# Kernel tuning notes

Hardware: AMD Instinct MI355X
Metric: run time of the kernel (lower is better)

## Reference

```python
import jax, jax.numpy as jnp
import numpy as np
from jax import lax

H = 128; N = 32768; D = 16; B = 256; E2 = N * D; L = 2; NC = 10
NPG = N // B  # nodes per graph


def _ln(x, g, b):
    m = jnp.mean(x, -1, keepdims=True)
    v = jnp.mean((x - m) ** 2, -1, keepdims=True)
    return (x - m) * lax.rsqrt(v + 1e-5) * g + b


def _lrelu(x):
    return jnp.where(x >= 0, x, 0.01 * x)


def _seg_mean(x, ids):
    s = jax.ops.segment_sum(x, ids, num_segments=B)
    c = jax.ops.segment_sum(jnp.ones((x.shape[0], 1), x.dtype), ids, num_segments=B)
    return s / c


def _lstm_agg(seq, Wih, Whh, bih, bhh):
    # seq: [N, D, H] neighbor message sequences; returns final hidden [N, H]
    n = seq.shape[0]
    h0 = jnp.zeros((n, H), seq.dtype)

    def step(carry, x):
        h, c = carry
        g = x @ Wih.T + bih + h @ Whh.T + bhh  # [N, 4H], gate order i,f,g,o (torch LSTM)
        i, f, gg, o = jnp.split(g, 4, axis=-1)
        c = jax.nn.sigmoid(f) * c + jax.nn.sigmoid(i) * jnp.tanh(gg)
        h = jax.nn.sigmoid(o) * jnp.tanh(c)
        return (h, c), None

    (h, _), _ = lax.scan(step, (h0, h0), jnp.swapaxes(seq, 0, 1))
    return h


def _gru(x, h, Wih, Whh, bih, bhh):
    gi = x @ Wih.T + bih
    gh = h @ Whh.T + bhh
    ir, iz, inn = jnp.split(gi, 3, axis=-1)
    hr, hz, hn = jnp.split(gh, 3, axis=-1)
    r = jax.nn.sigmoid(ir + hr)
    z = jax.nn.sigmoid(iz + hz)
    nn_ = jnp.tanh(inn + r * hn)
    return (1.0 - z) * nn_ + z * h


def _sage(fs, fd, nbr, Wih, Whh, bih, bhh, fsW, fsb, fnW, fnb):
    # SAGEConv with LSTM aggregator: fc_self(dst) + fc_neigh(lstm over neighbor feats)
    hn = _lstm_agg(fs[nbr], Wih, Whh, bih, bhh)  # [N, H]
    return fd @ fsW.T + fsb + hn @ fnW.T + fnb


def _forward(ints, fl):
    (act_ids, dur_ids, act2_ids, nbr_a2d, nbr_d2a, src2, dst2, graph_ids) = ints
    (emb_act, emb_dur, emb_act2, transform_W, transform_b,
     ggc_W, ggc_b, gru_Wih, gru_Whh, gru_bih, gru_bhh, hn_g, hn_b,
     lstm_Wih, lstm_Whh, lstm_bih, lstm_bhh, fcs_W, fcs_b, fcn_W, fcn_b,
     n1_g, n1_b, n3_g, n3_b,
     mh_W1, mh_b1, mh_W2, mh_b2, mo_W1, mo_b1, mo_W2, mo_b2,
     mlp_W1, mlp_b1, mlp_W2, mlp_b2, cls_W, cls_b) = fl

    # embedding lookups (dropout layers are identity in eval mode)
    h_act = emb_act[act_ids]
    h_dur = emb_dur[dur_ids]
    h_g2 = emb_act2[act2_ids]
    h_new = jnp.concatenate([h_g2, h_dur], axis=1) @ transform_W.T + transform_b

    # homo branch: GatedGraphConv (n_steps=2, 1 etype) + residual + LN + leaky_relu
    res = h_new
    hh = h_new
    for _ in range(2):
        m = hh @ ggc_W.T + ggc_b
        a = jax.ops.segment_sum(m[src2], dst2, num_segments=N)
        hh = _gru(a, hh, gru_Wih, gru_Whh, gru_bih, gru_bhh)
    h_new = _lrelu(_ln(hh + res, hn_g, hn_b))
    hg2_mean = _seg_mean(h_new, graph_ids)  # [B, H]

    # hetero branch: L layers of HeteroGraphConv(SAGEConv lstm) + norms + residuals
    ha, hd = h_act, h_dur
    for l in range(L):
        nd = _sage(ha, hd, nbr_a2d, lstm_Wih[l, 0], lstm_Whh[l, 0], lstm_bih[l, 0], lstm_bhh[l, 0],
                   fcs_W[l, 0], fcs_b[l, 0], fcn_W[l, 0], fcn_b[l, 0])
        na = _sage(hd, ha, nbr_d2a, lstm_Wih[l, 1], lstm_Whh[l, 1], lstm_bih[l, 1], lstm_bhh[l, 1],
                   fcs_W[l, 1], fcs_b[l, 1], fcn_W[l, 1], fcn_b[l, 1])
        na = _lrelu(_ln(na, n1_g[l, 0], n1_b[l, 0]))
        nd = _lrelu(_ln(nd, n1_g[l, 1], n1_b[l, 1]))
        ha = _lrelu(_ln(ha + na, n3_g[l, 0], n3_b[l, 0]))
        hd = _lrelu(_ln(hd + nd, n3_g[l, 1], n3_b[l, 1]))
    hg_mean = _seg_mean(ha, graph_ids) + _seg_mean(hd, graph_ids)  # sum over ntypes

    o1 = jax.nn.relu(jax.nn.relu(hg2_mean @ mo_W1.T + mo_b1) @ mo_W2.T + mo_b2)
    o2 = jax.nn.relu(jax.nn.relu(hg_mean @ mh_W1.T + mh_b1) @ mh_W2.T + mh_b2)
    hc = jnp.concatenate([o1, hg2_mean, o2, hg_mean], axis=1)  # [B, 4H]
    preds = jax.nn.relu(jax.nn.relu(hc @ mlp_W1.T + mlp_b1) @ mlp_W2.T + mlp_b2)
    return preds @ cls_W.T + cls_b  # [B, NC]


def setup_inputs() -> dict:
    key = jax.random.key(0)
    ks = iter(jax.random.split(key, 48))
    s = 1.0 / np.sqrt(H)

    def nrm(shape, sc=s):
        return jax.random.normal(next(ks), shape, jnp.float32) * sc

    inp = {}
    inp['act_ids'] = jax.random.randint(next(ks), (N,), 0, 30)
    inp['dur_ids'] = jax.random.randint(next(ks), (N,), 0, 1024)
    inp['act2_ids'] = jax.random.randint(next(ks), (N,), 0, 30)
    inp['nbr_a2d'] = jax.random.randint(next(ks), (N, D), 0, N)
    inp['nbr_d2a'] = jax.random.randint(next(ks), (N, D), 0, N)
    inp['src2'] = jax.random.randint(next(ks), (E2,), 0, N)
    inp['dst2'] = jax.random.randint(next(ks), (E2,), 0, N)
    inp['graph_ids'] = jnp.arange(N) // NPG

    inp['emb_act'] = nrm((30, H))
    inp['emb_dur'] = nrm((1024, H))
    inp['emb_act2'] = nrm((30, H))
    inp['transform_W'] = nrm((H, 2 * H), 1.0 / np.sqrt(2 * H))
    inp['transform_b'] = jnp.zeros((H,), jnp.float32)
    inp['ggc_W'] = nrm((H, H))
    inp['ggc_b'] = jnp.zeros((H,), jnp.float32)
    inp['gru_Wih'] = nrm((3 * H, H))
    inp['gru_Whh'] = nrm((3 * H, H))
    inp['gru_bih'] = jnp.zeros((3 * H,), jnp.float32)
    inp['gru_bhh'] = jnp.zeros((3 * H,), jnp.float32)
    inp['hn_g'] = jnp.ones((H,), jnp.float32)
    inp['hn_b'] = jnp.zeros((H,), jnp.float32)
    inp['lstm_Wih'] = nrm((L, 2, 4 * H, H))
    inp['lstm_Whh'] = nrm((L, 2, 4 * H, H))
    inp['lstm_bih'] = jnp.zeros((L, 2, 4 * H), jnp.float32)
    inp['lstm_bhh'] = jnp.zeros((L, 2, 4 * H), jnp.float32)
    inp['fcs_W'] = nrm((L, 2, H, H))
    inp['fcs_b'] = jnp.zeros((L, 2, H), jnp.float32)
    inp['fcn_W'] = nrm((L, 2, H, H))
    inp['fcn_b'] = jnp.zeros((L, 2, H), jnp.float32)
    inp['n1_g'] = jnp.ones((L, 2, H), jnp.float32)
    inp['n1_b'] = jnp.zeros((L, 2, H), jnp.float32)
    inp['n3_g'] = jnp.ones((L, 2, H), jnp.float32)
    inp['n3_b'] = jnp.zeros((L, 2, H), jnp.float32)
    inp['mh_W1'] = nrm((H, H)); inp['mh_b1'] = jnp.zeros((H,), jnp.float32)
    inp['mh_W2'] = nrm((H, H)); inp['mh_b2'] = jnp.zeros((H,), jnp.float32)
    inp['mo_W1'] = nrm((H, H)); inp['mo_b1'] = jnp.zeros((H,), jnp.float32)
    inp['mo_W2'] = nrm((H, H)); inp['mo_b2'] = jnp.zeros((H,), jnp.float32)
    inp['mlp_W1'] = nrm((2 * H, 4 * H), 1.0 / np.sqrt(4 * H))
    inp['mlp_b1'] = jnp.zeros((2 * H,), jnp.float32)
    inp['mlp_W2'] = nrm((H, 2 * H), 1.0 / np.sqrt(2 * H))
    inp['mlp_b2'] = jnp.zeros((H,), jnp.float32)
    inp['cls_W'] = nrm((NC, H))
    inp['cls_b'] = jnp.zeros((NC,), jnp.float32)
    return inp


def reference(act_ids, dur_ids, act2_ids, nbr_a2d, nbr_d2a, src2, dst2, graph_ids,
              emb_act, emb_dur, emb_act2, transform_W, transform_b,
              ggc_W, ggc_b, gru_Wih, gru_Whh, gru_bih, gru_bhh, hn_g, hn_b,
              lstm_Wih, lstm_Whh, lstm_bih, lstm_bhh, fcs_W, fcs_b, fcn_W, fcn_b,
              n1_g, n1_b, n3_g, n3_b,
              mh_W1, mh_b1, mh_W2, mh_b2, mo_W1, mo_b1, mo_W2, mo_b2,
              mlp_W1, mlp_b1, mlp_W2, mlp_b2, cls_W, cls_b):
    ints = (act_ids, dur_ids, act2_ids, nbr_a2d, nbr_d2a, src2, dst2, graph_ids)
    fl = (emb_act, emb_dur, emb_act2, transform_W, transform_b,
          ggc_W, ggc_b, gru_Wih, gru_Whh, gru_bih, gru_bhh, hn_g, hn_b,
          lstm_Wih, lstm_Whh, lstm_bih, lstm_bhh, fcs_W, fcs_b, fcn_W, fcn_b,
          n1_g, n1_b, n3_g, n3_b,
          mh_W1, mh_b1, mh_W2, mh_b2, mo_W1, mo_b1, mo_W2, mo_b2,
          mlp_W1, mlp_b1, mlp_W2, mlp_b2, cls_W, cls_b)
    return _forward(ints, fl)
```

## Files before the change

### kernel.cpp

```cpp
#include <hip/hip_runtime.h>
#include <hip/hip_fp16.h>
#include <math.h>

#define NN 32768
#define HH 128
#define DD 16
#define BB 256
#define E2N (NN*DD)
#define NF (NN*HH)

typedef __attribute__((ext_vector_type(4))) float f32x4;
typedef __attribute__((ext_vector_type(4))) unsigned short u16x4;
typedef __attribute__((ext_vector_type(8))) unsigned short u16x8;
typedef _Float16 f16x8 __attribute__((ext_vector_type(8)));

__device__ __forceinline__ float fsig(float x) {
  return __builtin_amdgcn_rcpf(1.0f + __builtin_amdgcn_exp2f(-1.442695041f*x));
}
__device__ __forceinline__ float ftanh(float x) {
  return 1.0f - 2.0f*__builtin_amdgcn_rcpf(1.0f + __builtin_amdgcn_exp2f(2.885390082f*x));
}

struct TDesc { const float* src; float* dst; int R; int C; };
struct TDescArr { TDesc d[8]; };

__global__ void transpose_many(TDescArr da) {
  TDesc t = da.d[blockIdx.y];
  int idx = blockIdx.x*256 + threadIdx.x;
  if (idx < t.R*t.C) {
    int r = idx / t.C, c = idx - r*t.C;
    t.dst[(size_t)c*t.R + r] = t.src[idx];
  }
}

__global__ void bias_sum_kernel(const float* __restrict__ bih, const float* __restrict__ bhh,
                                float* __restrict__ bsum) {
  int i = blockIdx.x*256 + threadIdx.x;
  if (i < 2048) bsum[i] = bih[i] + bhh[i];
}

__global__ void f32to16_kernel(const float* __restrict__ in, unsigned short* __restrict__ out) {
  int base = (blockIdx.x*256 + threadIdx.x) * 4;
  float4 v = *(const float4*)(in + base);
  u16x4 p;
  p[0] = __half_as_ushort(__float2half_rn(v.x));
  p[1] = __half_as_ushort(__float2half_rn(v.y));
  p[2] = __half_as_ushort(__float2half_rn(v.z));
  p[3] = __half_as_ushort(__float2half_rn(v.w));
  *(u16x4*)(out + base) = p;
}

__global__ void hist_kernel(const int* __restrict__ dst, int* __restrict__ cnt) {
  int e = blockIdx.x*256 + threadIdx.x;
  atomicAdd(&cnt[dst[e]], 1);
}

__global__ __launch_bounds__(1024) void scan_kernel(const int* __restrict__ cnt,
                                                    int* __restrict__ rowptr,
                                                    int* __restrict__ cursor) {
  __shared__ int part[1024];
  const int t = threadIdx.x;
  const int base = t*32;
  int loc[32];
  int s = 0;
#pragma unroll
  for (int k=0;k<32;++k){ loc[k]=s; s += cnt[base+k]; }
  part[t] = s;
  __syncthreads();
  for (int off=1; off<1024; off<<=1) {
    int v = (t>=off) ? part[t-off] : 0;
    __syncthreads();
    part[t] += v;
    __syncthreads();
  }
  int pbase = part[t] - s;
#pragma unroll
  for (int k=0;k<32;++k){ int v = pbase + loc[k]; rowptr[base+k]=v; cursor[base+k]=v; }
  if (t == 1023) rowptr[NN] = part[1023];
}

__global__ void fill_kernel(const int* __restrict__ src, const int* __restrict__ dst,
                            int* __restrict__ cursor, int* __restrict__ elist) {
  int e = blockIdx.x*256 + threadIdx.x;
  int p = atomicAdd(&cursor[dst[e]], 1);
  elist[p] = src[e];
}

__global__ __launch_bounds__(256) void gather_ggc(const float* __restrict__ m,
    const int* __restrict__ rowptr, const int* __restrict__ elist,
    float* __restrict__ a) {
  const int node = blockIdx.x*4 + (threadIdx.x>>6);
  const int lane = threadIdx.x & 63;
  const int s0 = rowptr[node], s1 = rowptr[node+1];
  float a0 = 0.0f, a1 = 0.0f;
  for (int e=s0; e<s1; ++e) {
    const float* mr = m + (size_t)elist[e]*128;
    a0 += mr[lane];
    a1 += mr[64+lane];
  }
  float* ar = a + (size_t)node*128;
  ar[lane] = a0;
  ar[64+lane] = a1;
}

__global__ void embed3_kernel(const int* __restrict__ a_ids, const int* __restrict__ d_ids,
                              const int* __restrict__ a2_ids,
                              const float* __restrict__ ea, const float* __restrict__ ed,
                              const float* __restrict__ ea2,
                              float* __restrict__ ha, float* __restrict__ hd,
                              float* __restrict__ hg2,
                              unsigned short* __restrict__ fs16a,
                              unsigned short* __restrict__ fs16d) {
  int idx = blockIdx.x*256 + threadIdx.x;
  int n = idx >> 7, j = idx & 127;
  int w = blockIdx.y;
  if (w == 0) {
    float v = ea[(size_t)a_ids[n]*128 + j];
    ha[idx] = v;
    fs16a[idx] = __half_as_ushort(__float2half_rn(v));
  } else if (w == 1) {
    float v = ed[(size_t)d_ids[n]*128 + j];
    hd[idx] = v;
    fs16d[idx] = __half_as_ushort(__float2half_rn(v));
  } else {
    hg2[idx] = ea2[(size_t)a2_ids[n]*128 + j];
  }
}

template<int BN, int ACT>
__global__ __launch_bounds__(256) void gemm_nt(
    const float* __restrict__ A0, const float* __restrict__ A1,
    const float* __restrict__ A2, const float* __restrict__ A3,
    int lda, const float* __restrict__ WT, const float* __restrict__ bias,
    float* __restrict__ C, int K, int beta)
{
  extern __shared__ float sm[];
  const int KP = K + 4;
  float* At = sm;
  float* Bc = sm + 32*KP;
  const int tid = threadIdx.x;
  const int m0 = blockIdx.x*32;
  const int ng = tid >> 5, cg = tid & 31;
  const int n0 = ng*4, c4 = cg*4;
  constexpr int G = BN/128;
  float acc[G][4][4];
#pragma unroll
  for (int g=0; g<G; ++g)
#pragma unroll
    for (int i=0;i<4;++i)
#pragma unroll
      for (int e=0;e<4;++e) acc[g][i][e] = 0.0f;

  const int nf4 = K >> 2;
  for (int idx = tid; idx < 32*nf4; idx += 256) {
    int row = idx / nf4;
    int kk = (idx - row*nf4) << 2;
    const float* Ap = (kk < 128) ? A0 : (kk < 256) ? A1 : (kk < 384) ? A2 : A3;
    float4 v = *(const float4*)(Ap + (size_t)(m0+row)*lda + (kk & 127));
    *(float4*)(At + row*KP + kk) = v;
  }
  const int nchunk = K >> 4;
  for (int kc = 0; kc < nchunk; ++kc) {
    __syncthreads();
    for (int idx = tid; idx < 16*(BN/4); idx += 256) {
      int kk = idx / (BN/4);
      int jq = idx - kk*(BN/4);
      *(float4*)(Bc + kk*BN + jq*4) = *(const float4*)(WT + (size_t)(kc*16+kk)*BN + jq*4);
    }
    __syncthreads();
    for (int k=0;k<16;++k) {
      const int kk = kc*16 + k;
      float av[4];
#pragma unroll
      for (int i=0;i<4;++i) av[i] = At[(n0+i)*KP + kk];
#pragma unroll
      for (int g=0; g<G; ++g) {
        float4 bv = *(const float4*)(Bc + k*BN + g*128 + c4);
        float bb[4] = {bv.x, bv.y, bv.z, bv.w};
#pragma unroll
        for (int i=0;i<4;++i)
#pragma unroll
          for (int e=0;e<4;++e)
            acc[g][i][e] += av[i]*bb[e];
      }
    }
  }
#pragma unroll
  for (int g=0; g<G; ++g) {
#pragma unroll
    for (int i=0;i<4;++i) {
      float* dst = C + (size_t)(m0+n0+i)*BN + g*128 + c4;
      float o[4];
#pragma unroll
      for (int e=0;e<4;++e) o[e] = acc[g][i][e];
      if (bias) {
#pragma unroll
        for (int e=0;e<4;++e) o[e] += bias[g*128 + c4 + e];
      }
      if (beta) {
        float4 p = *(const float4*)dst;
        o[0]+=p.x; o[1]+=p.y; o[2]+=p.z; o[3]+=p.w;
      }
      if (ACT==1) {
#pragma unroll
        for (int e=0;e<4;++e) o[e] = fmaxf(o[e], 0.0f);
      }
      *(float4*)dst = make_float4(o[0],o[1],o[2],o[3]);
    }
  }
}

__device__ __forceinline__ void stage_f16(const float* __restrict__ A, int rb, int tid,
                                          unsigned short* x16) {
  const int r = tid >> 3;
  const int cf = (tid & 7) * 16;
  const float* src = A + (size_t)(rb + r)*128 + cf;
  unsigned short* d = x16 + r*136 + cf;
#pragma unroll
  for (int q=0; q<4; ++q) {
    float4 v = *(const float4*)(src + q*4);
    u16x4 p;
    p[0] = __half_as_ushort(__float2half_rn(v.x));
    p[1] = __half_as_ushort(__float2half_rn(v.y));
    p[2] = __half_as_ushort(__float2half_rn(v.z));
    p[3] = __half_as_ushort(__float2half_rn(v.w));
    *(u16x4*)(d + q*4) = p;
  }
}

__global__ __launch_bounds__(512) void mgemm(
    const float* __restrict__ A, const unsigned short* __restrict__ W16,
    const float* __restrict__ bias, float* __restrict__ C, int BN, int ntpw)
{
  __shared__ unsigned short x16[64*136];
  const int tid = threadIdx.x;
  const int w = tid >> 6;
  const int lane = tid & 63;
  const int ln16 = lane & 15;
  const int lq = lane >> 4;
  const int rb = blockIdx.x * 64;
  stage_f16(A, rb, tid, x16);
  __syncthreads();

  for (int j=0; j<ntpw; ++j) {
    const int tile = w + j*8;
    f32x4 acc[4];
    f32x4 bv = *(const f32x4*)(bias + tile*16 + lq*4);
#pragma unroll
    for (int nt=0; nt<4; ++nt) acc[nt] = bv;
#pragma unroll
    for (int kt=0; kt<4; ++kt) {
      const int bo = kt*32 + lq*8;
      f16x8 bx[4];
#pragma unroll
      for (int nt=0; nt<4; ++nt)
        bx[nt] = *(const f16x8*)(x16 + (nt*16+ln16)*136 + bo);
      f16x8 ah = *(const f16x8*)(W16 + (size_t)(tile*16 + ln16)*128 + kt*32 + lq*8);
#pragma unroll
      for (int nt=0; nt<4; ++nt)
        acc[nt] = __builtin_amdgcn_mfma_f32_16x16x32_f16(ah, bx[nt], acc[nt], 0,0,0);
    }
#pragma unroll
    for (int nt=0; nt<4; ++nt) {
      f32x4 o = acc[nt];
      *(float4*)(C + (size_t)(rb + nt*16 + ln16)*BN + tile*16 + lq*4) =
          make_float4(o[0],o[1],o[2],o[3]);
    }
  }
}

__global__ __launch_bounds__(512) void mgemm2(
    const float* __restrict__ A1, const unsigned short* __restrict__ W1,
    const float* __restrict__ A2, const unsigned short* __restrict__ W2,
    const float* __restrict__ bias1, const float* __restrict__ bias2,
    float* __restrict__ C, float* __restrict__ C2, int wstride)
{
  __shared__ unsigned short x1[64*136];
  __shared__ unsigned short x2[64*136];
  const int tid = threadIdx.x;
  const int w = tid >> 6;
  const int lane = tid & 63;
  const int ln16 = lane & 15;
  const int lq = lane >> 4;
  const int rb = blockIdx.x * 64;
  stage_f16(A1, rb, tid, x1);
  stage_f16(A2, rb, tid, x2);
  __syncthreads();

  f32x4 acc[4];
  {
    f32x4 bv = *(const f32x4*)(bias1 + w*16 + lq*4);
    if (bias2) {
      f32x4 b2 = *(const f32x4*)(bias2 + w*16 + lq*4);
#pragma unroll
      for (int e=0;e<4;++e) bv[e] += b2[e];
    }
#pragma unroll
    for (int nt=0; nt<4; ++nt) acc[nt] = bv;
  }
#pragma unroll
  for (int p=0; p<2; ++p) {
    const unsigned short* x = p ? x2 : x1;
    const unsigned short* W = p ? W2 : W1;
#pragma unroll
    for (int kt=0; kt<4; ++kt) {
      const int bo = kt*32 + lq*8;
      f16x8 bx[4];
#pragma unroll
      for (int nt=0; nt<4; ++nt)
        bx[nt] = *(const f16x8*)(x + (nt*16+ln16)*136 + bo);
      f16x8 ah = *(const f16x8*)(W + (size_t)(w*16 + ln16)*wstride + kt*32 + lq*8);
#pragma unroll
      for (int nt=0; nt<4; ++nt)
        acc[nt] = __builtin_amdgcn_mfma_f32_16x16x32_f16(ah, bx[nt], acc[nt], 0,0,0);
    }
  }
#pragma unroll
  for (int nt=0; nt<4; ++nt) {
    f32x4 o = acc[nt];
    const size_t off = (size_t)(rb + nt*16 + ln16)*128 + w*16 + lq*4;
    *(float4*)(C + off) = make_float4(o[0],o[1],o[2],o[3]);
    if (C2) *(float4*)(C2 + off) = make_float4(o[0],o[1],o[2],o[3]);
  }
}

__global__ __launch_bounds__(512) void gru_fused(
    const float* __restrict__ abuf, float* __restrict__ hh,
    const unsigned short* __restrict__ GI16, const unsigned short* __restrict__ GH16,
    const float* __restrict__ bih, const float* __restrict__ bhh)
{
  __shared__ unsigned short x16[64*136];
  __shared__ unsigned short h16[64*136];
  const int tid = threadIdx.x;
  const int w = tid >> 6;
  const int lane = tid & 63;
  const int ln16 = lane & 15;
  const int lq = lane >> 4;
  const int rb = blockIdx.x * 64;
  stage_f16(abuf, rb, tid, x16);
  stage_f16(hh, rb, tid, h16);
  __syncthreads();

  f32x4 rr[4], zz[4], nn_[4];
#pragma unroll
  for (int j=0; j<3; ++j) {
    const int tile = w + j*8;
    f32x4 ai[4], ag[4];
    f32x4 bi = *(const f32x4*)(bih + tile*16 + lq*4);
    f32x4 bg = *(const f32x4*)(bhh + tile*16 + lq*4);
#pragma unroll
    for (int nt=0; nt<4; ++nt) { ai[nt] = bi; ag[nt] = bg; }
#pragma unroll
    for (int kt=0; kt<4; ++kt) {
      const int bo = kt*32 + lq*8;
      f16x8 bx[4], bh_[4];
#pragma unroll
      for (int nt=0; nt<4; ++nt) {
        bx[nt] = *(const f16x8*)(x16 + (nt*16+ln16)*136 + bo);
        bh_[nt] = *(const f16x8*)(h16 + (nt*16+ln16)*136 + bo);
      }
      const size_t co = (size_t)(tile*16 + ln16)*128 + kt*32 + lq*8;
      f16x8 aI = *(const f16x8*)(GI16 + co);
      f16x8 aH = *(const f16x8*)(GH16 + co);
#pragma unroll
      for (int nt=0; nt<4; ++nt) {
        ai[nt] = __builtin_amdgcn_mfma_f32_16x16x32_f16(aI, bx[nt], ai[nt], 0,0,0);
        ag[nt] = __builtin_amdgcn_mfma_f32_16x16x32_f16(aH, bh_[nt], ag[nt], 0,0,0);
      }
    }
#pragma unroll
    for (int nt=0; nt<4; ++nt) {
#pragma unroll
      for (int e=0; e<4; ++e) {
        if (j == 0)      rr[nt][e] = fsig(ai[nt][e] + ag[nt][e]);
        else if (j == 1) zz[nt][e] = fsig(ai[nt][e] + ag[nt][e]);
        else             nn_[nt][e] = ftanh(ai[nt][e] + rr[nt][e]*ag[nt][e]);
      }
    }
  }
#pragma unroll
  for (int nt=0; nt<4; ++nt) {
    float* hp = hh + (size_t)(rb + nt*16 + ln16)*128 + w*16 + lq*4;
    float4 ho = *(const float4*)hp;
    float hv[4] = {ho.x, ho.y, ho.z, ho.w};
    float o[4];
#pragma unroll
    for (int e=0; e<4; ++e)
      o[e] = (1.0f - zz[nt][e])*nn_[nt][e] + zz[nt][e]*hv[e];
    *(float4*)hp = make_float4(o[0],o[1],o[2],o[3]);
  }
}

__global__ __launch_bounds__(512) void lstm_fused6(
    float* __restrict__ hL,
    const unsigned short* __restrict__ fs16a, const unsigned short* __restrict__ fs16d,
    const int* __restrict__ nbrA, const int* __restrict__ nbrD,
    const unsigned short* __restrict__ WI0, const unsigned short* __restrict__ WH0,
    const unsigned short* __restrict__ WI1, const unsigned short* __restrict__ WH1,
    const float* __restrict__ bsum0, const float* __restrict__ bsum1)
{
  __shared__ unsigned short xb[64*132];
  __shared__ unsigned short hb[64*132];
  const int tid = threadIdx.x;
  const int w = tid >> 6;
  const int lane = tid & 63;
  const int ln16 = lane & 15;
  const int lq = lane >> 4;
  const int b = blockIdx.x;
  const bool dir = (b >= 512);
  const int nb = (dir ? (b - 512) : b) * 64;
  const unsigned short* fs16 = dir ? fs16d : fs16a;
  const int* nbr = dir ? nbrD : nbrA;
  const unsigned short* WI = dir ? WI1 : WI0;
  const unsigned short* WH = dir ? WH1 : WH0;
  const float* bsum = dir ? bsum1 : bsum0;

  const int gr = tid >> 3;
  const int gc = (tid & 7) * 16;
  const int* nrow = nbr + (size_t)(nb + gr)*DD;

  f32x4 bias[4];
#pragma unroll
  for (int g=0; g<4; ++g)
    bias[g] = *(const f32x4*)(bsum + g*128 + w*16 + lq*4);

  f32x4 cst[4];
#pragma unroll
  for (int nt=0; nt<4; ++nt)
#pragma unroll
    for (int e=0; e<4; ++e) cst[nt][e] = 0.0f;

  u16x8 xg0, xg1;
  {
    int gidx = nrow[0];
    const unsigned short* src = fs16 + (size_t)gidx*128 + gc;
    xg0 = *(const u16x8*)(src);
    xg1 = *(const u16x8*)(src + 8);
    unsigned short* d = xb + gr*132 + gc;
    *(u16x8*)d = xg0;
    *(u16x8*)(d+8) = xg1;
  }
  int gnext = nrow[1];

#pragma unroll 1
  for (int t=0; t<16; ++t) {
    __syncthreads();

    f32x4 racc[4][4];
#pragma unroll
    for (int g=0; g<4; ++g)
#pragma unroll
      for (int nt=0; nt<4; ++nt)
        racc[g][nt] = bias[g];

#pragma unroll
    for (int kt=0; kt<4; ++kt) {
      const int bo = kt*32 + lq*8;
      f16x8 bx[4];
#pragma unroll
      for (int nt=0; nt<4; ++nt)
        bx[nt] = *(const f16x8*)(xb + (nt*16+ln16)*132 + bo);
#pragma unroll
      for (int g=0; g<4; ++g) {
        f16x8 aI = *(const f16x8*)(WI + (size_t)(g*128 + w*16 + ln16)*128 + kt*32 + lq*8);
#pragma unroll
        for (int nt=0; nt<4; ++nt)
          racc[g][nt] = __builtin_amdgcn_mfma_f32_16x16x32_f16(aI, bx[nt], racc[g][nt], 0,0,0);
      }
    }
    if (t < 15) {
      const unsigned short* src = fs16 + (size_t)gnext*128 + gc;
      xg0 = *(const u16x8*)(src);
      xg1 = *(const u16x8*)(src + 8);
      if (t < 14) gnext = nrow[t+2];
    }
    if (t > 0) {
#pragma unroll
      for (int kt=0; kt<4; ++kt) {
        const int bo = kt*32 + lq*8;
        f16x8 bh[4];
#pragma unroll
        for (int nt=0; nt<4; ++nt)
          bh[nt] = *(const f16x8*)(hb + (nt*16+ln16)*132 + bo);
#pragma unroll
        for (int g=0; g<4; ++g) {
          f16x8 aH = *(const f16x8*)(WH + (size_t)(g*128 + w*16 + ln16)*128 + kt*32 + lq*8);
#pragma unroll
          for (int nt=0; nt<4; ++nt)
            racc[g][nt] = __builtin_amdgcn_mfma_f32_16x16x32_f16(aH, bh[nt], racc[g][nt], 0,0,0);
        }
      }
    }
    __syncthreads();

#pragma unroll
    for (int nt=0; nt<4; ++nt) {
      float hv[4];
#pragma unroll
      for (int e=0; e<4; ++e) {
        float ig = fsig(racc[0][nt][e]);
        float fg = fsig(racc[1][nt][e]);
        float gg = ftanh(racc[2][nt][e]);
        float og = fsig(racc[3][nt][e]);
        float cc = fg*cst[nt][e] + ig*gg;
        cst[nt][e] = cc;
        hv[e] = og*ftanh(cc);
      }
      const int node = nt*16 + ln16;
      const int col = w*16 + lq*4;
      if (t < 15) {
        u16x4 hw;
#pragma unroll
        for (int e=0; e<4; ++e) hw[e] = __half_as_ushort(__float2half_rn(hv[e]));
        *(u16x4*)(hb + node*132 + col) = hw;
      } else {
        *(float4*)(hL + (size_t)((dir?NN:0) + nb + node)*128 + col) =
            make_float4(hv[0], hv[1], hv[2], hv[3]);
      }
    }
    if (t < 15) {
      unsigned short* d = xb + gr*132 + gc;
      *(u16x8*)d = xg0;
      *(u16x8*)(d+8) = xg1;
    }
  }
}

__global__ void ln_lrelu_kernel(float* __restrict__ out, const float* __restrict__ x,
                                const float* __restrict__ add,
                                const float* __restrict__ g, const float* __restrict__ b) {
  int n = blockIdx.x, j = threadIdx.x;
  size_t base = (size_t)n*128;
  float v = x[base+j];
  if (add) v += add[base+j];
  __shared__ float sh[4];
  float s = v;
#pragma unroll
  for (int m=32; m>=1; m>>=1) s += __shfl_xor(s, m, 64);
  if ((j&63)==0) sh[j>>6] = s;
  __syncthreads();
  float mean = (sh[0]+sh[1]) * 0.0078125f;
  float d = v - mean;
  float q = d*d;
#pragma unroll
  for (int m=32; m>=1; m>>=1) q += __shfl_xor(q, m, 64);
  if ((j&63)==0) sh[2+(j>>6)] = q;
  __syncthreads();
  float var = (sh[2]+sh[3]) * 0.0078125f;
  float y = d * rsqrtf(var + 1e-5f) * g[j] + b[j];
  out[base+j] = (y >= 0.0f) ? y : 0.01f*y;
}

__global__ void ln13_kernel(float* __restrict__ h, const float* __restrict__ nsrc,
                            const float* __restrict__ g1, const float* __restrict__ b1,
                            const float* __restrict__ g3, const float* __restrict__ b3,
                            unsigned short* __restrict__ out16) {
  int n = blockIdx.x, j = threadIdx.x;
  size_t base = (size_t)n*128;
  __shared__ float sh[4];
  float v = nsrc[base+j];
  float s = v;
#pragma unroll
  for (int m=32; m>=1; m>>=1) s += __shfl_xor(s, m, 64);
  if ((j&63)==0) sh[j>>6] = s;
  __syncthreads();
  float mean = (sh[0]+sh[1]) * 0.0078125f;
  float d = v - mean;
  float q = d*d;
#pragma unroll
  for (int m=32; m>=1; m>>=1) q += __shfl_xor(q, m, 64);
  if ((j&63)==0) sh[2+(j>>6)] = q;
  __syncthreads();
  float var = (sh[2]+sh[3]) * 0.0078125f;
  float y1 = d * rsqrtf(var + 1e-5f) * g1[j] + b1[j];
  y1 = (y1 >= 0.0f) ? y1 : 0.01f*y1;
  __syncthreads();
  float u = h[base+j] + y1;
  s = u;
#pragma unroll
  for (int m=32; m>=1; m>>=1) s += __shfl_xor(s, m, 64);
  if ((j&63)==0) sh[j>>6] = s;
  __syncthreads();
  mean = (sh[0]+sh[1]) * 0.0078125f;
  d = u - mean;
  q = d*d;
#pragma unroll
  for (int m=32; m>=1; m>>=1) q += __shfl_xor(q, m, 64);
  if ((j&63)==0) sh[2+(j>>6)] = q;
  __syncthreads();
  var = (sh[2]+sh[3]) * 0.0078125f;
  float y3 = d * rsqrtf(var + 1e-5f) * g3[j] + b3[j];
  float o = (y3 >= 0.0f) ? y3 : 0.01f*y3;
  h[base+j] = o;
  if (out16) out16[base+j] = __half_as_ushort(__float2half_rn(o));
}

__global__ void segmean_kernel(float* __restrict__ out, const float* __restrict__ x,
                               const float* __restrict__ y) {
  int b = blockIdx.x, j = threadIdx.x;
  float s = 0.0f;
  for (int r=0; r<128; ++r) {
    size_t n = (size_t)(b*128 + r)*128 + j;
    s += x[n];
    if (y) s += y[n];
  }
  out[(size_t)b*128 + j] = s * 0.0078125f;
}

__global__ void cls_kernel(float* __restrict__ out, const float* __restrict__ h2,
                           const float* __restrict__ Wc, const float* __restrict__ bc) {
  int gid = blockIdx.x*256 + threadIdx.x;
  if (gid >= BB*10) return;
  int mrow = gid/10, c = gid - mrow*10;
  const float* arow = h2 + (size_t)mrow*128;
  const float* wrow = Wc + (size_t)c*128;
  float s = bc[c];
  for (int k=0;k<128;++k) s += arow[k]*wrow[k];
  out[gid] = s;
}

__global__ void bail_kernel(float* out, float v) {
  if (threadIdx.x==0 && blockIdx.x==0) out[0] = v;
}

extern "C" void kernel_launch(void* const* d_in, const int* in_sizes, int n_in,
                              void* d_out, int out_size, void* d_ws, size_t ws_size,
                              hipStream_t stream)
{
  const int* act_ids  = (const int*)d_in[0];
  const int* dur_ids  = (const int*)d_in[1];
  const int* act2_ids = (const int*)d_in[2];
  const int* nbr_a2d  = (const int*)d_in[3];
  const int* nbr_d2a  = (const int*)d_in[4];
  const int* src2     = (const int*)d_in[5];
  const int* dst2     = (const int*)d_in[6];
  const float* emb_act     = (const float*)d_in[8];
  const float* emb_dur     = (const float*)d_in[9];
  const float* emb_act2    = (const float*)d_in[10];
  const float* transform_W = (const float*)d_in[11];
  const float* transform_b = (const float*)d_in[12];
  const float* ggc_W   = (const float*)d_in[13];
  const float* ggc_b   = (const float*)d_in[14];
  const float* gru_Wih = (const float*)d_in[15];
  const float* gru_Whh = (const float*)d_in[16];
  const float* gru_bih = (const float*)d_in[17];
  const float* gru_bhh = (const float*)d_in[18];
  const float* hn_g    = (const float*)d_in[19];
  const float* hn_b    = (const float*)d_in[20];
  const float* lstm_Wih = (const float*)d_in[21];
  const float* lstm_Whh = (const float*)d_in[22];
  const float* lstm_bih = (const float*)d_in[23];
  const float* lstm_bhh = (const float*)d_in[24];
  const float* fcs_W = (const float*)d_in[25];
  const float* fcs_b = (const float*)d_in[26];
  const float* fcn_W = (const float*)d_in[27];
  const float* fcn_b = (const float*)d_in[28];
  const float* n1_g = (const float*)d_in[29];
  const float* n1_b = (const float*)d_in[30];
  const float* n3_g = (const float*)d_in[31];
  const float* n3_b = (const float*)d_in[32];
  const float* mh_W1 = (const float*)d_in[33];
  const float* mh_b1 = (const float*)d_in[34];
  const float* mh_W2 = (const float*)d_in[35];
  const float* mh_b2 = (const float*)d_in[36];
  const float* mo_W1 = (const float*)d_in[37];
  const float* mo_b1 = (const float*)d_in[38];
  const float* mo_W2 = (const float*)d_in[39];
  const float* mo_b2 = (const float*)d_in[40];
  const float* mlp_W1 = (const float*)d_in[41];
  const float* mlp_b1 = (const float*)d_in[42];
  const float* mlp_W2 = (const float*)d_in[43];
  const float* mlp_b2 = (const float*)d_in[44];
  const float* cls_W = (const float*)d_in[45];
  const float* cls_b = (const float*)d_in[46];

  float* ws = (float*)d_ws;
  float* ha   = ws;
  float* hd   = ws + (size_t)NF;
  float* hg2  = ws + 2*(size_t)NF;
  float* res  = ws + 3*(size_t)NF;
  float* hh   = ws + 4*(size_t)NF;
  float* SCR  = ws + 5*(size_t)NF;
  float* mb   = SCR;
  float* abuf = SCR + (size_t)NF;
  float* hnf  = mb;
  float* hLb  = SCR + 8*(size_t)NF;
  float* SMALL = ws + 15*(size_t)NF;
  float* hg2m = SMALL;
  float* hgm  = SMALL + 32768;
  float* o1b  = SMALL + 65536;
  float* o2b  = SMALL + 98304;
  float* t1b  = SMALL + 131072;
  float* t2b  = SMALL + 163840;
  float* h1b  = SMALL + 196608;
  float* h2b  = SMALL + 262144;
  float* bsum = SMALL + 294912;
  float* WTb  = SMALL + 296960;
  const size_t NEED_BYTES = (size_t)(15*(size_t)NF + 296960 + 1032192) * 4;
  if (ws_size < NEED_BYTES) {
    hipMemsetAsync(d_out, 0, (size_t)out_size*sizeof(float), stream);
    bail_kernel<<<1,64,0,stream>>>((float*)d_out, (float)ws_size);
    return;
  }
  float* na = hg2;
  float* nd = res;
  unsigned short* fs16a = (unsigned short*)(SCR + 2*(size_t)NF);
  unsigned short* fs16d = fs16a + (size_t)NF;
  int* csr_cnt    = (int*)(SCR + 3*(size_t)NF);
  int* csr_rowptr = csr_cnt + NN;
  int* csr_cursor = csr_rowptr + NN + 2;
  int* csr_elist  = csr_cursor + NN;

  const int O_TRANSFORM = 0;
  const int O_SPLIT    = 147456;
  const int O_SPLIT2   = 409600;
  const int O_MH1      = 802816;
  const int O_MH2      = 819200;
  const int O_MO1      = 835584;
  const int O_MO2      = 851968;
  const int O_MLP1     = 868352;
  const int O_MLP2     = 999424;

  unsigned short* T16 = (unsigned short*)(WTb + O_TRANSFORM);
  unsigned short* WI16 = (unsigned short*)(WTb + O_SPLIT);
  unsigned short* WH16 = WI16 + 4*65536;

  unsigned short* SP2 = (unsigned short*)(WTb + O_SPLIT2);
  unsigned short* GGC16 = SP2;
  unsigned short* GIH16 = GGC16 + 16384;
  unsigned short* GHH16 = GIH16 + 49152;
  unsigned short* FCS16 = GHH16 + 49152;
  unsigned short* FCN16 = FCS16 + 65536;

  TDescArr da;
  int di = 0;
  auto addT = [&](const float* s, float* d, int R, int C){ da.d[di].src=s; da.d[di].dst=d; da.d[di].R=R; da.d[di].C=C; ++di; };
  addT(mh_W1, WTb + O_MH1, 128, 128);
  addT(mh_W2, WTb + O_MH2, 128, 128);
  addT(mo_W1, WTb + O_MO1, 128, 128);
  addT(mo_W2, WTb + O_MO2, 128, 128);
  addT(mlp_W1, WTb + O_MLP1, 256, 512);
  addT(mlp_W2, WTb + O_MLP2, 128, 256);
  transpose_many<<<dim3(512, di), 256, 0, stream>>>(da);
  bias_sum_kernel<<<8, 256, 0, stream>>>(lstm_bih, lstm_bhh, bsum);
  f32to16_kernel<<<(4*512*128)/1024, 256, 0, stream>>>(lstm_Wih, WI16);
  f32to16_kernel<<<(4*512*128)/1024, 256, 0, stream>>>(lstm_Whh, WH16);
  f32to16_kernel<<<32768/1024, 256, 0, stream>>>(transform_W, T16);
  f32to16_kernel<<<16384/1024, 256, 0, stream>>>(ggc_W, GGC16);
  f32to16_kernel<<<49152/1024, 256, 0, stream>>>(gru_Wih, GIH16);
  f32to16_kernel<<<49152/1024, 256, 0, stream>>>(gru_Whh, GHH16);
  f32to16_kernel<<<65536/1024, 256, 0, stream>>>(fcs_W, FCS16);
  f32to16_kernel<<<65536/1024, 256, 0, stream>>>(fcn_W, FCN16);
  hipMemsetAsync(csr_cnt, 0, (size_t)NN*sizeof(int), stream);
  hist_kernel<<<E2N/256, 256, 0, stream>>>(dst2, csr_cnt);
  scan_kernel<<<1, 1024, 0, stream>>>(csr_cnt, csr_rowptr, csr_cursor);
  fill_kernel<<<E2N/256, 256, 0, stream>>>(src2, dst2, csr_cursor, csr_elist);

  auto smemK = [](int K, int BN){ return (size_t)(32*(K+4) + 16*BN)*4; };
  const int gB = BB/32;
  const int gM = NN/64;

  embed3_kernel<<<dim3(NF/256, 3), 256, 0, stream>>>(act_ids, dur_ids, act2_ids,
      emb_act, emb_dur, emb_act2, ha, hd, hg2, fs16a, fs16d);
  mgemm2<<<gM, 512, 0, stream>>>(hg2, T16, hd, T16 + 128,
      transform_b, nullptr, res, hh, 256);

  for (int it=0; it<2; ++it) {
    mgemm<<<gM, 512, 0, stream>>>(hh, GGC16, ggc_b, mb, 128, 1);
    gather_ggc<<<NN/4, 256, 0, stream>>>(mb, csr_rowptr, csr_elist, abuf);
    gru_fused<<<gM, 512, 0, stream>>>(abuf, hh, GIH16, GHH16, gru_bih, gru_bhh);
  }
  ln_lrelu_kernel<<<NN, 128, 0, stream>>>(hnf, hh, res, hn_g, hn_b);
  segmean_kernel<<<BB, 128, 0, stream>>>(hg2m, hnf, nullptr);

  for (int l=0; l<2; ++l) {
    const int i0 = l*2 + 0, i1 = l*2 + 1;
    lstm_fused6<<<1024, 512, 0, stream>>>(hLb, fs16a, fs16d, nbr_a2d, nbr_d2a,
        WI16 + i0*65536, WH16 + i0*65536,
        WI16 + i1*65536, WH16 + i1*65536,
        bsum + i0*512, bsum + i1*512);

    mgemm2<<<gM, 512, 0, stream>>>(hd, FCS16 + i0*16384,
        hLb, FCN16 + i0*16384,
        fcs_b + i0*128, fcn_b + i0*128, nd, nullptr, 128);
    mgemm2<<<gM, 512, 0, stream>>>(ha, FCS16 + i1*16384,
        hLb + (size_t)NN*128, FCN16 + i1*16384,
        fcs_b + i1*128, fcn_b + i1*128, na, nullptr, 128);
    ln13_kernel<<<NN, 128, 0, stream>>>(ha, na, n1_g + i0*128, n1_b + i0*128,
        n3_g + i0*128, n3_b + i0*128, (l==0) ? fs16a : nullptr);
    ln13_kernel<<<NN, 128, 0, stream>>>(hd, nd, n1_g + i1*128, n1_b + i1*128,
        n3_g + i1*128, n3_b + i1*128, (l==0) ? fs16d : nullptr);
  }
  segmean_kernel<<<BB, 128, 0, stream>>>(hgm, ha, hd);

  gemm_nt<128,1><<<gB, 256, smemK(128,128), stream>>>(hg2m, nullptr, nullptr, nullptr, 128,
      WTb + O_MO1, mo_b1, t1b, 128, 0);
  gemm_nt<128,1><<<gB, 256, smemK(128,128), stream>>>(t1b, nullptr, nullptr, nullptr, 128,
      WTb + O_MO2, mo_b2, o1b, 128, 0);
  gemm_nt<128,1><<<gB, 256, smemK(128,128), stream>>>(hgm, nullptr, nullptr, nullptr, 128,
      WTb + O_MH1, mh_b1, t2b, 128, 0);
  gemm_nt<128,1><<<gB, 256, smemK(128,128), stream>>>(t2b, nullptr, nullptr, nullptr, 128,
      WTb + O_MH2, mh_b2, o2b, 128, 0);
  gemm_nt<256,0><<<gB, 256, smemK(256,256), stream>>>(o1b, hg2m, nullptr, nullptr, 128,
      WTb + O_MLP1, nullptr, h1b, 256, 0);
  gemm_nt<256,1><<<gB, 256, smemK(256,256), stream>>>(o2b, hgm, nullptr, nullptr, 128,
      WTb + O_MLP1 + 256*256, mlp_b1, h1b, 256, 1);
  gemm_nt<128,1><<<gB, 256, smemK(256,128), stream>>>(h1b, h1b + 128, nullptr, nullptr, 256,
      WTb + O_MLP2, mlp_b2, h2b, 256, 0);
  cls_kernel<<<10, 256, 0, stream>>>((float*)d_out, h2b, cls_W, cls_b);
}
```

Baseline: 1.583 ms.

## Store GGC messages in fp16 and batch weight conversions into one launch

The GGC message GEMM now writes its output as fp16 instead of fp32, and the edge gather reads those fp16 rows and accumulates in fp32. This halves the bytes read in the random-access neighbor gather over 524k edges. It also merges eight fp32-to-fp16 weight conversion launches into a single descriptor-driven launch. The cost is an extra rounding of the messages to fp16, which slightly increases numerical error.

New measurement: 1.564 ms (median of 2 runs). Within noise of the previous version (-1.2%).

```diff
diff --git a/kernel.cpp b/kernel.cpp
--- a/kernel.cpp
+++ b/kernel.cpp
@@ -39,15 +39,21 @@
   if (i < 2048) bsum[i] = bih[i] + bhh[i];
 }
 
-__global__ void f32to16_kernel(const float* __restrict__ in, unsigned short* __restrict__ out) {
+struct CDesc { const float* src; unsigned short* dst; int n; };
+struct CDescArr { CDesc d[8]; };
+
+__global__ void f32to16_many(CDescArr da) {
+  CDesc c = da.d[blockIdx.y];
   int base = (blockIdx.x*256 + threadIdx.x) * 4;
-  float4 v = *(const float4*)(in + base);
-  u16x4 p;
-  p[0] = __half_as_ushort(__float2half_rn(v.x));
-  p[1] = __half_as_ushort(__float2half_rn(v.y));
-  p[2] = __half_as_ushort(__float2half_rn(v.z));
-  p[3] = __half_as_ushort(__float2half_rn(v.w));
-  *(u16x4*)(out + base) = p;
+  if (base < c.n) {
+    float4 v = *(const float4*)(c.src + base);
+    u16x4 p;
+    p[0] = __half_as_ushort(__float2half_rn(v.x));
+    p[1] = __half_as_ushort(__float2half_rn(v.y));
+    p[2] = __half_as_ushort(__float2half_rn(v.z));
+    p[3] = __half_as_ushort(__float2half_rn(v.w));
+    *(u16x4*)(c.dst + base) = p;
+  }
 }
 
 __global__ void hist_kernel(const int* __restrict__ dst, int* __restrict__ cnt) {
@@ -86,7 +92,7 @@
   elist[p] = src[e];
 }
 
-__global__ __launch_bounds__(256) void gather_ggc(const float* __restrict__ m,
+__global__ __launch_bounds__(256) void gather_ggc(const unsigned short* __restrict__ m16,
     const int* __restrict__ rowptr, const int* __restrict__ elist,
     float* __restrict__ a) {
   const int node = blockIdx.x*4 + (threadIdx.x>>6);
@@ -94,9 +100,9 @@
   const int s0 = rowptr[node], s1 = rowptr[node+1];
   float a0 = 0.0f, a1 = 0.0f;
   for (int e=s0; e<s1; ++e) {
-    const float* mr = m + (size_t)elist[e]*128;
-    a0 += mr[lane];
-    a1 += mr[64+lane];
+    const unsigned short* mr = m16 + (size_t)elist[e]*128;
+    a0 += __half2float(__ushort_as_half(mr[lane]));
+    a1 += __half2float(__ushort_as_half(mr[64+lane]));
   }
   float* ar = a + (size_t)node*128;
   ar[lane] = a0;
@@ -228,9 +234,9 @@
   }
 }
 
-__global__ __launch_bounds__(512) void mgemm(
+__global__ __launch_bounds__(512) void mgemm_h16(
     const float* __restrict__ A, const unsigned short* __restrict__ W16,
-    const float* __restrict__ bias, float* __restrict__ C, int BN, int ntpw)
+    const float* __restrict__ bias, unsigned short* __restrict__ C16)
 {
   __shared__ unsigned short x16[64*136];
   const int tid = threadIdx.x;
@@ -242,30 +248,29 @@
   stage_f16(A, rb, tid, x16);
   __syncthreads();
 
-  for (int j=0; j<ntpw; ++j) {
-    const int tile = w + j*8;
-    f32x4 acc[4];
-    f32x4 bv = *(const f32x4*)(bias + tile*16 + lq*4);
-#pragma unroll
-    for (int nt=0; nt<4; ++nt) acc[nt] = bv;
-#pragma unroll
-    for (int kt=0; kt<4; ++kt) {
-      const int bo = kt*32 + lq*8;
-      f16x8 bx[4];
-#pragma unroll
-      for (int nt=0; nt<4; ++nt)
-        bx[nt] = *(const f16x8*)(x16 + (nt*16+ln16)*136 + bo);
-      f16x8 ah = *(const f16x8*)(W16 + (size_t)(tile*16 + ln16)*128 + kt*32 + lq*8);
-#pragma unroll
-      for (int nt=0; nt<4; ++nt)
-        acc[nt] = __builtin_amdgcn_mfma_f32_16x16x32_f16(ah, bx[nt], acc[nt], 0,0,0);
-    }
-#pragma unroll
-    for (int nt=0; nt<4; ++nt) {
-      f32x4 o = acc[nt];
-      *(float4*)(C + (size_t)(rb + nt*16 + ln16)*BN + tile*16 + lq*4) =
-          make_float4(o[0],o[1],o[2],o[3]);
-    }
+  f32x4 acc[4];
+  f32x4 bv = *(const f32x4*)(bias + w*16 + lq*4);
+#pragma unroll
+  for (int nt=0; nt<4; ++nt) acc[nt] = bv;
+#pragma unroll
+  for (int kt=0; kt<4; ++kt) {
+    const int bo = kt*32 + lq*8;
+    f16x8 bx[4];
+#pragma unroll
+    for (int nt=0; nt<4; ++nt)
+      bx[nt] = *(const f16x8*)(x16 + (nt*16+ln16)*136 + bo);
+    f16x8 ah = *(const f16x8*)(W16 + (size_t)(w*16 + ln16)*128 + kt*32 + lq*8);
+#pragma unroll
+    for (int nt=0; nt<4; ++nt)
+      acc[nt] = __builtin_amdgcn_mfma_f32_16x16x32_f16(ah, bx[nt], acc[nt], 0,0,0);
+  }
+#pragma unroll
+  for (int nt=0; nt<4; ++nt) {
+    f32x4 o = acc[nt];
+    u16x4 p;
+#pragma unroll
+    for (int e=0;e<4;++e) p[e] = __half_as_ushort(__float2half_rn(o[e]));
+    *(u16x4*)(C16 + (size_t)(rb + nt*16 + ln16)*128 + w*16 + lq*4) = p;
   }
 }
 
@@ -681,9 +686,8 @@
   float* res  = ws + 3*(size_t)NF;
   float* hh   = ws + 4*(size_t)NF;
   float* SCR  = ws + 5*(size_t)NF;
-  float* mb   = SCR;
   float* abuf = SCR + (size_t)NF;
-  float* hnf  = mb;
+  float* hnf  = SCR;
   float* hLb  = SCR + 8*(size_t)NF;
   float* SMALL = ws + 15*(size_t)NF;
   float* hg2m = SMALL;
@@ -704,6 +708,7 @@
   }
   float* na = hg2;
   float* nd = res;
+  unsigned short* mb16 = (unsigned short*)SCR;
   unsigned short* fs16a = (unsigned short*)(SCR + 2*(size_t)NF);
   unsigned short* fs16d = fs16a + (size_t)NF;
   int* csr_cnt    = (int*)(SCR + 3*(size_t)NF);
@@ -743,14 +748,20 @@
   addT(mlp_W2, WTb + O_MLP2, 128, 256);
   transpose_many<<<dim3(512, di), 256, 0, stream>>>(da);
   bias_sum_kernel<<<8, 256, 0, stream>>>(lstm_bih, lstm_bhh, bsum);
-  f32to16_kernel<<<(4*512*128)/1024, 256, 0, stream>>>(lstm_Wih, WI16);
-  f32to16_kernel<<<(4*512*128)/1024, 256, 0, stream>>>(lstm_Whh, WH16);
-  f32to16_kernel<<<32768/1024, 256, 0, stream>>>(transform_W, T16);
-  f32to16_kernel<<<16384/1024, 256, 0, stream>>>(ggc_W, GGC16);
-  f32to16_kernel<<<49152/1024, 256, 0, stream>>>(gru_Wih, GIH16);
-  f32to16_kernel<<<49152/1024, 256, 0, stream>>>(gru_Whh, GHH16);
-  f32to16_kernel<<<65536/1024, 256, 0, stream>>>(fcs_W, FCS16);
-  f32to16_kernel<<<65536/1024, 256, 0, stream>>>(fcn_W, FCN16);
+
+  CDescArr ca;
+  int ci = 0;
+  auto addC = [&](const float* s, unsigned short* d, int n){ ca.d[ci].src=s; ca.d[ci].dst=d; ca.d[ci].n=n; ++ci; };
+  addC(lstm_Wih, WI16, 4*512*128);
+  addC(lstm_Whh, WH16, 4*512*128);
+  addC(transform_W, T16, 32768);
+  addC(ggc_W, GGC16, 16384);
+  addC(gru_Wih, GIH16, 49152);
+  addC(gru_Whh, GHH16, 49152);
+  addC(fcs_W, FCS16, 65536);
+  addC(fcn_W, FCN16, 65536);
+  f32to16_many<<<dim3(256, ci), 256, 0, stream>>>(ca);
+
   hipMemsetAsync(csr_cnt, 0, (size_t)NN*sizeof(int), stream);
   hist_kernel<<<E2N/256, 256, 0, stream>>>(dst2, csr_cnt);
   scan_kernel<<<1, 1024, 0, stream>>>(csr_cnt, csr_rowptr, csr_cursor);
@@ -766,8 +777,8 @@
       transform_b, nullptr, res, hh, 256);
 
   for (int it=0; it<2; ++it) {
-    mgemm<<<gM, 512, 0, stream>>>(hh, GGC16, ggc_b, mb, 128, 1);
-    gather_ggc<<<NN/4, 256, 0, stream>>>(mb, csr_rowptr, csr_elist, abuf);
+    mgemm_h16<<<gM, 512, 0, stream>>>(hh, GGC16, ggc_b, mb16);
+    gather_ggc<<<NN/4, 256, 0, stream>>>(mb16, csr_rowptr, csr_elist, abuf);
     gru_fused<<<gM, 512, 0, stream>>>(abuf, hh, GIH16, GHH16, gru_bih, gru_bhh);
   }
   ln_lrelu_kernel<<<NN, 128, 0, stream>>>(hnf, hh, res, hn_g, hn_b);
```
